# Optimization experiments

Hardware: AMD Instinct MI355X
Metric: run time of the kernel (lower is better)

## Reference

```python
import jax, jax.numpy as jnp
import numpy as np
import math

B, S, D, H = 8, 2048, 1024, 16
DH = D // H  # attention head size = 64

def setup_inputs() -> dict:
    key = jax.random.key(0)
    ks = jax.random.split(key, 10)
    s = 1.0 / math.sqrt(D)
    return {
        "hidden_states": jax.random.normal(ks[0], (B, S, D), dtype=jnp.float32),
        "attention_mask": jnp.zeros((B, 1, S), dtype=jnp.float32),
        "Wq": jax.random.normal(ks[1], (D, D), dtype=jnp.float32) * s,
        "bq": jnp.zeros((D,), dtype=jnp.float32),
        "Wqa": jax.random.normal(ks[2], (D, H), dtype=jnp.float32) * s,
        "bqa": jnp.zeros((H,), dtype=jnp.float32),
        "Wk": jax.random.normal(ks[3], (D, D), dtype=jnp.float32) * s,
        "bk": jnp.zeros((D,), dtype=jnp.float32),
        "Wt": jax.random.normal(ks[4], (D, D), dtype=jnp.float32) * s,
        "bt": jnp.zeros((D,), dtype=jnp.float32),
    }

def reference(hidden_states, attention_mask, Wq, bq, Wqa, bqa, Wk, bk, Wt, bt):
    scale = 1.0 / math.sqrt(DH)
    q = hidden_states @ Wq + bq                      # [B,S,D] mixed_query_layer
    k = hidden_states @ Wk + bk                      # [B,S,D] mixed_key_layer
    # query attention logits -> [B,H,S]
    q_score = jnp.swapaxes(q @ Wqa + bqa, 1, 2) * scale + attention_mask
    q_weight = jax.nn.softmax(q_score, axis=-1)      # [B,H,S]
    ql = jnp.swapaxes(q.reshape(B, S, H, DH), 1, 2)  # [B,H,S,DH]
    kl = jnp.swapaxes(k.reshape(B, S, H, DH), 1, 2)  # [B,H,S,DH]
    pooled_q = jnp.einsum('bhs,bhsd->bhd', q_weight, ql)          # [B,H,DH]
    qk_score = jnp.einsum('bhsd,bhd->bhs', kl, pooled_q) * scale + attention_mask
    qk_weight = jax.nn.softmax(qk_score, axis=-1)                 # [B,H,S]
    pooled_k = jnp.einsum('bhs,bhsd->bhd', qk_weight, kl)         # [B,H,DH]
    weighted = pooled_k[:, :, None, :] * ql                       # [B,H,S,DH]
    weighted = jnp.swapaxes(weighted, 1, 2).reshape(B, S, D)      # [B,S,D]
    out = weighted @ Wt + bt + q                                  # transform + residual to query
    return out
```

## Files before the change

kernel.cpp:

```cpp
#include <hip/hip_runtime.h>
#include <hip/hip_bf16.h>
#include <math.h>

#define BB 8
#define SS 2048
#define DD 1024
#define HH 16
#define DHH 64
#define NROWS (BB*SS)
#define QSLICE ((size_t)BB * HH * SS)

typedef unsigned short u16;
typedef __attribute__((ext_vector_type(8))) __bf16 bf16x8;
typedef __attribute__((ext_vector_type(4))) float f32x4;

__device__ __forceinline__ u16 f2bf(float f) {
    union { float f; unsigned u; } v; v.f = f;
    unsigned r = v.u + 0x7fffu + ((v.u >> 16) & 1u);
    return (u16)(r >> 16);
}
__device__ __forceinline__ float bf2f(u16 b) {
    union { unsigned u; float f; } v; v.u = ((unsigned)b) << 16;
    return v.f;
}

__device__ __forceinline__ void load_lds16(const void* g, void* l) {
    __builtin_amdgcn_global_load_lds(
        (const __attribute__((address_space(1))) unsigned int*)g,
        (__attribute__((address_space(3))) unsigned int*)l,
        16, 0, 0);
}

#define BAR() do { asm volatile("" ::: "memory"); \
                   __builtin_amdgcn_s_barrier();  \
                   asm volatile("" ::: "memory"); } while (0)

__global__ __launch_bounds__(256) void cast_bf16_kernel(const float* __restrict__ in,
                                                        u16* __restrict__ out, int n4) {
    int i = blockIdx.x * 256 + threadIdx.x;
    if (i >= n4) return;
    float4 v = ((const float4*)in)[i];
    ushort4 o;
    o.x = f2bf(v.x); o.y = f2bf(v.y); o.z = f2bf(v.z); o.w = f2bf(v.w);
    ((ushort4*)out)[i] = o;
}

__global__ __launch_bounds__(256) void transpose_cast_kernel(const float* __restrict__ W,
                                                             u16* __restrict__ WT) {
    __shared__ float tile[32][33];
    int m0 = blockIdx.x * 32, k0 = blockIdx.y * 32;
    int tx = threadIdx.x & 31, ty = threadIdx.x >> 5;
    #pragma unroll
    for (int i = 0; i < 4; i++) {
        int kk = ty + i * 8;
        tile[kk][tx] = W[(k0 + kk) * DD + m0 + tx];
    }
    __syncthreads();
    #pragma unroll
    for (int i = 0; i < 4; i++) {
        int mm = ty + i * 8;
        WT[(m0 + mm) * DD + k0 + tx] = f2bf(tile[tx][mm]);
    }
}

__global__ __launch_bounds__(256) void wqa_transpose_kernel(const float* __restrict__ Wqa,
                                                            u16* __restrict__ WqaT) {
    int i = blockIdx.x * 256 + threadIdx.x;
    int h = i >> 10, k = i & 1023;
    WqaT[i] = f2bf(Wqa[k * HH + h]);
}

template<int MODE>
__global__ __launch_bounds__(512, 2)
void gemm256_kernel(const u16* __restrict__ A, const u16* __restrict__ BT,
                    const float* __restrict__ b0, const float* __restrict__ b1,
                    const u16* __restrict__ res, float* __restrict__ Cf,
                    u16* __restrict__ C0, u16* __restrict__ C1) {
    __shared__ u16 smem[69632];
    const int by = blockIdx.y;
    const int row0 = blockIdx.x * 256;
    const int bcol0 = by * 256;
    const int colg0 = (MODE == 1) ? (bcol0 & 1023) : bcol0;
    const float* bias = (MODE == 1 && by >= 4) ? b1 : b0;
    u16* Cb = (MODE == 1 && by >= 4) ? C1 : C0;

    const int t = threadIdx.x;
    const int w = t >> 6, lane = t & 63;
    const int wm = w >> 2, wn = w & 3;
    const int m16 = lane & 15, quad = lane >> 4;

    f32x4 acc[8][4];
    #pragma unroll
    for (int i = 0; i < 8; i++)
        #pragma unroll
        for (int j = 0; j < 4; j++)
            acc[i][j] = (f32x4){0.f, 0.f, 0.f, 0.f};

    const int srow = t >> 3;
    const int scol = ((t & 7) ^ (srow & 7)) * 8;
    const u16* Ag = A + (size_t)(row0 + srow) * DD + scol;
    const u16* Bg = BT + (size_t)(bcol0 + srow) * DD + scol;

    auto STAGE_H = [&](int ktile, int mat, int half) {
        if (ktile >= 16) return;
        const int buf = ktile & 1;
        const int k0 = ktile * 64;
        const u16* g = mat ? Bg : Ag;
        u16* s = smem + mat * 32768 + buf * 16384;
        #pragma unroll
        for (int j = 0; j < 2; ++j)
            load_lds16(g + k0 + (size_t)(half * 128 + j * 64) * DD,
                       s + half * 8192 + j * 4096 + t * 8);
    };

    STAGE_H(0, 0, 0); STAGE_H(0, 0, 1); STAGE_H(0, 1, 0); STAGE_H(0, 1, 1);
    STAGE_H(1, 0, 0);
    asm volatile("s_waitcnt vmcnt(2)" ::: "memory");
    BAR();

    for (int kt = 0; kt < 16; ++kt) {
        const int cur = kt & 1;
        const u16* sAc = smem + cur * 16384;
        const u16* sBc = smem + 32768 + cur * 16384;
        bf16x8 af[4][2], bfr[4][2];

        #pragma unroll
        for (int mi = 0; mi < 4; ++mi)
            #pragma unroll
            for (int ks = 0; ks < 2; ++ks)
                af[mi][ks] = *(const bf16x8*)&sAc[(wm * 128 + mi * 16 + m16) * 64 +
                                                 (((ks * 4 + quad) ^ (m16 & 7)) * 8)];
        #pragma unroll
        for (int ni = 0; ni < 2; ++ni)
            #pragma unroll
            for (int ks = 0; ks < 2; ++ks)
                bfr[ni][ks] = *(const bf16x8*)&sBc[(wn * 64 + ni * 16 + m16) * 64 +
                                                   (((ks * 4 + quad) ^ (m16 & 7)) * 8)];
        STAGE_H(kt + 1, 0, 1);
        BAR();
        __builtin_amdgcn_s_setprio(1);
        #pragma unroll
        for (int mi = 0; mi < 4; ++mi)
            #pragma unroll
            for (int ni = 0; ni < 2; ++ni)
                #pragma unroll
                for (int ks = 0; ks < 2; ++ks)
                    acc[mi][ni] = __builtin_amdgcn_mfma_f32_16x16x32_bf16(
                        bfr[ni][ks], af[mi][ks], acc[mi][ni], 0, 0, 0);
        __builtin_amdgcn_s_setprio(0);
        BAR();

        #pragma unroll
        for (int ni = 2; ni < 4; ++ni)
            #pragma unroll
            for (int ks = 0; ks < 2; ++ks)
                bfr[ni][ks] = *(const bf16x8*)&sBc[(wn * 64 + ni * 16 + m16) * 64 +
                                                   (((ks * 4 + quad) ^ (m16 & 7)) * 8)];
        STAGE_H(kt + 1, 1, 0);
        BAR();
        __builtin_amdgcn_s_setprio(1);
        #pragma unroll
        for (int mi = 0; mi < 4; ++mi)
            #pragma unroll
            for (int ni = 2; ni < 4; ++ni)
                #pragma unroll
                for (int ks = 0; ks < 2; ++ks)
                    acc[mi][ni] = __builtin_amdgcn_mfma_f32_16x16x32_bf16(
                        bfr[ni][ks], af[mi][ks], acc[mi][ni], 0, 0, 0);
        __builtin_amdgcn_s_setprio(0);
        BAR();

        #pragma unroll
        for (int mi = 0; mi < 4; ++mi)
            #pragma unroll
            for (int ks = 0; ks < 2; ++ks)
                af[mi][ks] = *(const bf16x8*)&sAc[(wm * 128 + (4 + mi) * 16 + m16) * 64 +
                                                 (((ks * 4 + quad) ^ (m16 & 7)) * 8)];
        STAGE_H(kt + 1, 1, 1);
        BAR();
        __builtin_amdgcn_s_setprio(1);
        #pragma unroll
        for (int mi = 0; mi < 4; ++mi)
            #pragma unroll
            for (int ni = 0; ni < 2; ++ni)
                #pragma unroll
                for (int ks = 0; ks < 2; ++ks)
                    acc[4 + mi][ni] = __builtin_amdgcn_mfma_f32_16x16x32_bf16(
                        bfr[ni][ks], af[mi][ks], acc[4 + mi][ni], 0, 0, 0);
        __builtin_amdgcn_s_setprio(0);
        BAR();

        STAGE_H(kt + 2, 0, 0);
        BAR();
        __builtin_amdgcn_s_setprio(1);
        #pragma unroll
        for (int mi = 0; mi < 4; ++mi)
            #pragma unroll
            for (int ni = 2; ni < 4; ++ni)
                #pragma unroll
                for (int ks = 0; ks < 2; ++ks)
                    acc[4 + mi][ni] = __builtin_amdgcn_mfma_f32_16x16x32_bf16(
                        bfr[ni][ks], af[mi][ks], acc[4 + mi][ni], 0, 0, 0);
        __builtin_amdgcn_s_setprio(0);
        if (kt < 14) asm volatile("s_waitcnt vmcnt(2)" ::: "memory");
        else         asm volatile("s_waitcnt vmcnt(0)" ::: "memory");
        BAR();
    }

    u16* sC = smem;
    #pragma unroll
    for (int mi = 0; mi < 8; ++mi) {
        const int lrow = wm * 128 + mi * 16 + m16;
        #pragma unroll
        for (int ni = 0; ni < 4; ++ni) {
            const int lcol = wn * 64 + ni * 16 + quad * 4;
            const float4 bv = *(const float4*)&bias[colg0 + lcol];
            if (MODE == 1) {
                ushort4 o;
                o.x = f2bf(acc[mi][ni][0] + bv.x);
                o.y = f2bf(acc[mi][ni][1] + bv.y);
                o.z = f2bf(acc[mi][ni][2] + bv.z);
                o.w = f2bf(acc[mi][ni][3] + bv.w);
                *(ushort4*)&sC[(size_t)lrow * 272 + lcol] = o;
            } else {
                const size_t idx = (size_t)(row0 + lrow) * DD + colg0 + lcol;
                const ushort4 rv = *(const ushort4*)&res[idx];
                float4 o;
                o.x = acc[mi][ni][0] + bv.x + bf2f(rv.x);
                o.y = acc[mi][ni][1] + bv.y + bf2f(rv.y);
                o.z = acc[mi][ni][2] + bv.z + bf2f(rv.z);
                o.w = acc[mi][ni][3] + bv.w + bf2f(rv.w);
                *(float4*)&Cf[idx] = o;
            }
        }
    }
    if (MODE == 1) {
        __syncthreads();
        #pragma unroll
        for (int it = 0; it < 16; ++it) {
            const int r = it * 16 + (t >> 5);
            const int c = t & 31;
            uint4 v = *(const uint4*)&sC[(size_t)r * 272 + c * 8];
            *(uint4*)&Cb[(size_t)(row0 + r) * DD + colg0 + c * 8] = v;
        }
    }
}

__global__ __launch_bounds__(256)
void qscore_mfma_kernel(const u16* __restrict__ qbf, const u16* __restrict__ WqaT,
                        float* __restrict__ qraw) {
    int w = threadIdx.x >> 6, lane = threadIdx.x & 63;
    int row0 = blockIdx.x * 64 + w * 16;
    int kbase = blockIdx.y * 256;
    int m16 = lane & 15, quad = lane >> 4;
    f32x4 acc = (f32x4){0.f, 0.f, 0.f, 0.f};
    const u16* ap = qbf + (size_t)(row0 + m16) * DD + kbase + quad * 8;
    const u16* bp = WqaT + (size_t)m16 * DD + kbase + quad * 8;
    #pragma unroll
    for (int kk = 0; kk < 256; kk += 32) {
        bf16x8 a = *(const bf16x8*)(ap + kk);
        bf16x8 b = *(const bf16x8*)(bp + kk);
        acc = __builtin_amdgcn_mfma_f32_16x16x32_bf16(a, b, acc, 0, 0, 0);
    }
    #pragma unroll
    for (int r = 0; r < 4; r++) {
        int grow = row0 + quad * 4 + r;
        int b = grow >> 11, sidx = grow & 2047;
        qraw[((size_t)(blockIdx.y * BB + b) * HH + m16) * SS + sidx] = acc[r];
    }
}

template<bool EPI>
__global__ __launch_bounds__(256)
void softmax_kernel(float* __restrict__ score, const float* __restrict__ bqa,
                    const float* __restrict__ mask) {
    int bh = blockIdx.x;
    int b = bh >> 4, h = bh & 15;
    float* srow = score + ((size_t)bh << 11);
    __shared__ float rm[4], rs[4];
    int t = threadIdx.x;

    float v[8];
    float m = -1e30f;
    #pragma unroll
    for (int i = 0; i < 8; i++) {
        int off = t + i * 256;
        float x;
        if (EPI) {
            x = srow[off] + srow[off + QSLICE] + srow[off + 2 * QSLICE] + srow[off + 3 * QSLICE];
            x = (x + bqa[h]) * 0.125f + mask[b * SS + off];
        } else {
            x = srow[off];
        }
        v[i] = x; m = fmaxf(m, x);
    }
    #pragma unroll
    for (int off = 32; off; off >>= 1) m = fmaxf(m, __shfl_xor(m, off));
    if ((t & 63) == 0) rm[t >> 6] = m;
    __syncthreads();
    m = fmaxf(fmaxf(rm[0], rm[1]), fmaxf(rm[2], rm[3]));

    float sum = 0.f;
    #pragma unroll
    for (int i = 0; i < 8; i++) { v[i] = __expf(v[i] - m); sum += v[i]; }
    #pragma unroll
    for (int off = 32; off; off >>= 1) sum += __shfl_xor(sum, off);
    if ((t & 63) == 0) rs[t >> 6] = sum;
    __syncthreads();
    float inv = 1.0f / (rs[0] + rs[1] + rs[2] + rs[3]);
    #pragma unroll
    for (int i = 0; i < 8; i++) srow[t + i * 256] = v[i] * inv;
}

__global__ __launch_bounds__(256)
void pool_kernel(const float* __restrict__ w, const u16* __restrict__ X,
                 float* __restrict__ pooled) {
    int b = blockIdx.x;
    int s0 = blockIdx.y * 32;
    int t = threadIdx.x;
    int wid = t >> 6, lane = t & 63;
    int h = lane >> 2;
    __shared__ float sw[16 * 33];
    __shared__ float pr[4][64 * 17];
    {
        int hh = t >> 4, si = t & 15;
        const float* wr = w + ((size_t)(b * HH + hh) << 11) + s0;
        sw[hh * 33 + si] = wr[si];
        sw[hh * 33 + si + 16] = wr[si + 16];
    }
    __syncthreads();
    float acc[16];
    #pragma unroll
    for (int j = 0; j < 16; j++) acc[j] = 0.f;
    const u16* xbase = X + ((size_t)(b * SS + s0 + wid * 8) << 10) + lane * 16;
    #pragma unroll
    for (int rr = 0; rr < 8; rr++) {
        float ws = sw[h * 33 + wid * 8 + rr];
        const uint4* xp = (const uint4*)(xbase + (size_t)rr * DD);
        uint4 x0 = xp[0], x1 = xp[1];
        unsigned xw[8] = {x0.x, x0.y, x0.z, x0.w, x1.x, x1.y, x1.z, x1.w};
        #pragma unroll
        for (int i2 = 0; i2 < 8; i2++) {
            union { unsigned u; float f; } lo, hi;
            lo.u = xw[i2] << 16; hi.u = xw[i2] & 0xffff0000u;
            acc[2 * i2]     += ws * lo.f;
            acc[2 * i2 + 1] += ws * hi.f;
        }
    }
    #pragma unroll
    for (int j = 0; j < 16; j++) pr[wid][lane * 17 + j] = acc[j];
    __syncthreads();
    #pragma unroll
    for (int i = 0; i < 4; i++) {
        int idx = t + i * 256;
        int l2 = idx >> 4, j2 = idx & 15;
        float v = pr[0][l2 * 17 + j2] + pr[1][l2 * 17 + j2] +
                  pr[2][l2 * 17 + j2] + pr[3][l2 * 17 + j2];
        int od = (l2 >> 2) * 64 + (l2 & 3) * 16 + j2;
        atomicAdd(&pooled[b * DD + od], v);
    }
}

__global__ __launch_bounds__(256)
void qkscore_kernel(const u16* __restrict__ kbf, const float* __restrict__ pq,
                    const float* __restrict__ mask, float* __restrict__ qkscore) {
    int row = blockIdx.x * 4 + (threadIdx.x >> 6);
    int lane = threadIdx.x & 63;
    int b = row >> 11, s = row & 2047;
    int h = lane >> 2, dp = lane & 3;
    const u16* kp = kbf + (size_t)row * DD + h * 64 + dp * 16;
    const float* pqp = pq + (size_t)(b * HH + h) * 64 + dp * 16;
    const uint4* kp4 = (const uint4*)kp;
    uint4 ka = kp4[0], kb4 = kp4[1];
    unsigned kw[8] = {ka.x, ka.y, ka.z, ka.w, kb4.x, kb4.y, kb4.z, kb4.w};
    float acc = 0.f;
    #pragma unroll
    for (int i = 0; i < 8; i++) {
        union { unsigned u; float f; } lo, hi;
        lo.u = kw[i] << 16;
        hi.u = kw[i] & 0xffff0000u;
        acc += lo.f * pqp[2 * i] + hi.f * pqp[2 * i + 1];
    }
    acc += __shfl_xor(acc, 1);
    acc += __shfl_xor(acc, 2);
    if (dp == 0) qkscore[(size_t)(b * HH + h) * SS + s] = acc * 0.125f + mask[b * SS + s];
}

__global__ __launch_bounds__(256)
void weighted_kernel(const u16* __restrict__ qbf, const float* __restrict__ pk,
                     u16* __restrict__ wout) {
    int i = blockIdx.x * 256 + threadIdx.x;
    int row = i >> 8;
    int c0 = (i & 255) << 2;
    int b = row >> 11;
    int h = c0 >> 6, d = c0 & 63;
    ushort4 qv = ((const ushort4*)qbf)[i];
    const float4 pv = *(const float4*)(pk + (size_t)(b * HH + h) * 64 + d);
    ushort4 o;
    o.x = f2bf(bf2f(qv.x) * pv.x); o.y = f2bf(bf2f(qv.y) * pv.y);
    o.z = f2bf(bf2f(qv.z) * pv.z); o.w = f2bf(bf2f(qv.w) * pv.w);
    ((ushort4*)wout)[i] = o;
}

extern "C" void kernel_launch(void* const* d_in, const int* in_sizes, int n_in,
                              void* d_out, int out_size, void* d_ws, size_t ws_size,
                              hipStream_t stream) {
    const float* hs   = (const float*)d_in[0];
    const float* mask = (const float*)d_in[1];
    const float* Wq   = (const float*)d_in[2];
    const float* bq   = (const float*)d_in[3];
    const float* Wqa  = (const float*)d_in[4];
    const float* bqa  = (const float*)d_in[5];
    const float* Wk   = (const float*)d_in[6];
    const float* bk   = (const float*)d_in[7];
    const float* Wt   = (const float*)d_in[8];
    const float* bt   = (const float*)d_in[9];
    float* out = (float*)d_out;

    char* ws = (char*)d_ws;
    u16*   hs_bf = (u16*)ws;   ws += (size_t)NROWS * DD * 2;
    u16*   WqT   = (u16*)ws;   ws += (size_t)DD * DD * 2;
    u16*   WkT   = (u16*)ws;   ws += (size_t)DD * DD * 2;
    u16*   WtT   = (u16*)ws;   ws += (size_t)DD * DD * 2;
    u16*   WqaT  = (u16*)ws;   ws += (size_t)HH * DD * 2;
    u16*   q_bf  = (u16*)ws;   ws += (size_t)NROWS * DD * 2;
    u16*   k_bf  = (u16*)ws;   ws += (size_t)NROWS * DD * 2;
    float* qraw  = (float*)ws; ws += QSLICE * 4 * 4;
    float* qksc  = (float*)ws; ws += (size_t)BB * HH * SS * 4;
    float* pq    = (float*)ws; ws += (size_t)BB * HH * 64 * 4;
    float* pk    = (float*)ws; ws += (size_t)BB * HH * 64 * 4;
    u16*   wbf   = hs_bf;

    int n4 = NROWS * DD / 4;
    cast_bf16_kernel<<<n4 / 256, 256, 0, stream>>>(hs, hs_bf, n4);
    transpose_cast_kernel<<<dim3(32, 32), 256, 0, stream>>>(Wq, WqT);
    transpose_cast_kernel<<<dim3(32, 32), 256, 0, stream>>>(Wk, WkT);
    transpose_cast_kernel<<<dim3(32, 32), 256, 0, stream>>>(Wt, WtT);
    wqa_transpose_kernel<<<HH * DD / 256, 256, 0, stream>>>(Wqa, WqaT);

    hipMemsetAsync(pq, 0, (size_t)BB * HH * 64 * 4, stream);
    hipMemsetAsync(pk, 0, (size_t)BB * HH * 64 * 4, stream);

    gemm256_kernel<1><<<dim3(NROWS / 256, 8), 512, 0, stream>>>(
        hs_bf, WqT, bq, bk, nullptr, nullptr, q_bf, k_bf);

    qscore_mfma_kernel<<<dim3(NROWS / 64, 4), 256, 0, stream>>>(q_bf, WqaT, qraw);
    softmax_kernel<true><<<BB * HH, 256, 0, stream>>>(qraw, bqa, mask);
    pool_kernel<<<dim3(BB, SS / 32), 256, 0, stream>>>(qraw, q_bf, pq);
    qkscore_kernel<<<NROWS / 4, 256, 0, stream>>>(k_bf, pq, mask, qksc);
    softmax_kernel<false><<<BB * HH, 256, 0, stream>>>(qksc, nullptr, nullptr);
    pool_kernel<<<dim3(BB, SS / 32), 256, 0, stream>>>(qksc, k_bf, pk);
    weighted_kernel<<<n4 / 256, 256, 0, stream>>>(q_bf, pk, wbf);

    gemm256_kernel<2><<<dim3(NROWS / 256, 4), 512, 0, stream>>>(
        wbf, WtT, bt, nullptr, q_bf, out, nullptr, nullptr);
}
```

Baseline: 309.6 us.

## Fold pooled-key scaling into per-batch Wt, fuse q-score into QK GEMM, merge prep kernels

Replaces the elementwise weighted = pk*q pass with a per-batch scaled copy of WtT, so the output GEMM reads q_bf directly against batch-specific weights. The q@Wqa logits are now computed in the QK GEMM epilogue from the bf16 q tile already in LDS, which removes the separate qscore kernel and its reread of q. The casts, transposes and memsets are merged into one prep kernel to cut launch overhead. In exchange it writes 8 scaled weight copies (16 MB), and the output GEMM's B-operand reuse across batches drops.

```diff
diff --git a/kernel.cpp b/kernel.cpp
--- a/kernel.cpp
+++ b/kernel.cpp
@@ -35,39 +35,57 @@
                    __builtin_amdgcn_s_barrier();  \
                    asm volatile("" ::: "memory"); } while (0)
 
-__global__ __launch_bounds__(256) void cast_bf16_kernel(const float* __restrict__ in,
-                                                        u16* __restrict__ out, int n4) {
-    int i = blockIdx.x * 256 + threadIdx.x;
-    if (i >= n4) return;
-    float4 v = ((const float4*)in)[i];
-    ushort4 o;
-    o.x = f2bf(v.x); o.y = f2bf(v.y); o.z = f2bf(v.z); o.w = f2bf(v.w);
-    ((ushort4*)out)[i] = o;
-}
-
-__global__ __launch_bounds__(256) void transpose_cast_kernel(const float* __restrict__ W,
-                                                             u16* __restrict__ WT) {
+__global__ __launch_bounds__(256)
+void prep_kernel(const float* __restrict__ hs, u16* __restrict__ hs_bf,
+                 const float* __restrict__ Wq, u16* __restrict__ WqT,
+                 const float* __restrict__ Wk, u16* __restrict__ WkT,
+                 const float* __restrict__ Wt, u16* __restrict__ WtT,
+                 const float* __restrict__ Wqa, u16* __restrict__ WqaT,
+                 float* __restrict__ pq, float* __restrict__ pk) {
     __shared__ float tile[32][33];
-    int m0 = blockIdx.x * 32, k0 = blockIdx.y * 32;
-    int tx = threadIdx.x & 31, ty = threadIdx.x >> 5;
-    #pragma unroll
-    for (int i = 0; i < 4; i++) {
-        int kk = ty + i * 8;
-        tile[kk][tx] = W[(k0 + kk) * DD + m0 + tx];
-    }
-    __syncthreads();
-    #pragma unroll
-    for (int i = 0; i < 4; i++) {
-        int mm = ty + i * 8;
-        WT[(m0 + mm) * DD + k0 + tx] = f2bf(tile[tx][mm]);
-    }
-}
-
-__global__ __launch_bounds__(256) void wqa_transpose_kernel(const float* __restrict__ Wqa,
-                                                            u16* __restrict__ WqaT) {
-    int i = blockIdx.x * 256 + threadIdx.x;
-    int h = i >> 10, k = i & 1023;
-    WqaT[i] = f2bf(Wqa[k * HH + h]);
+    const int bid = blockIdx.x;
+    const int t = threadIdx.x;
+    if (bid < 16384) {
+        int i = bid * 256 + t;
+        float4 v = ((const float4*)hs)[i];
+        ushort4 o;
+        o.x = f2bf(v.x); o.y = f2bf(v.y); o.z = f2bf(v.z); o.w = f2bf(v.w);
+        ((ushort4*)hs_bf)[i] = o;
+        return;
+    }
+    if (bid < 19456) {
+        int rel = bid - 16384;
+        const float* W; u16* WT;
+        if (rel < 1024)      { W = Wq; WT = WqT; }
+        else if (rel < 2048) { W = Wk; WT = WkT; rel -= 1024; }
+        else                 { W = Wt; WT = WtT; rel -= 2048; }
+        int m0 = (rel & 31) * 32, k0 = (rel >> 5) * 32;
+        int tx = t & 31, ty = t >> 5;
+        #pragma unroll
+        for (int i = 0; i < 4; i++) {
+            int kk = ty + i * 8;
+            tile[kk][tx] = W[(k0 + kk) * DD + m0 + tx];
+        }
+        __syncthreads();
+        #pragma unroll
+        for (int i = 0; i < 4; i++) {
+            int mm = ty + i * 8;
+            WT[(m0 + mm) * DD + k0 + tx] = f2bf(tile[tx][mm]);
+        }
+        return;
+    }
+    if (bid < 19520) {
+        int i = (bid - 19456) * 256 + t;
+        int h = i >> 10, k = i & 1023;
+        WqaT[i] = f2bf(Wqa[k * HH + h]);
+        return;
+    }
+    {
+        int i = (bid - 19520) * 256 + t;
+        float4 z = {0.f, 0.f, 0.f, 0.f};
+        if (i < 2048) ((float4*)pq)[i] = z;
+        else          ((float4*)pk)[i - 2048] = z;
+    }
 }
 
 template<int MODE>
@@ -75,7 +93,8 @@
 void gemm256_kernel(const u16* __restrict__ A, const u16* __restrict__ BT,
                     const float* __restrict__ b0, const float* __restrict__ b1,
                     const u16* __restrict__ res, float* __restrict__ Cf,
-                    u16* __restrict__ C0, u16* __restrict__ C1) {
+                    u16* __restrict__ C0, u16* __restrict__ C1,
+                    const u16* __restrict__ WqaT, float* __restrict__ qraw) {
     __shared__ u16 smem[69632];
     const int by = blockIdx.y;
     const int row0 = blockIdx.x * 256;
@@ -83,6 +102,7 @@
     const int colg0 = (MODE == 1) ? (bcol0 & 1023) : bcol0;
     const float* bias = (MODE == 1 && by >= 4) ? b1 : b0;
     u16* Cb = (MODE == 1 && by >= 4) ? C1 : C0;
+    const u16* BTb = (MODE == 2) ? BT + ((size_t)(row0 >> 11) << 20) : BT;
 
     const int t = threadIdx.x;
     const int w = t >> 6, lane = t & 63;
@@ -99,7 +119,7 @@
     const int srow = t >> 3;
     const int scol = ((t & 7) ^ (srow & 7)) * 8;
     const u16* Ag = A + (size_t)(row0 + srow) * DD + scol;
-    const u16* Bg = BT + (size_t)(bcol0 + srow) * DD + scol;
+    const u16* Bg = BTb + (size_t)(bcol0 + srow) * DD + scol;
 
     auto STAGE_H = [&](int ktile, int mat, int half) {
         if (ktile >= 16) return;
@@ -243,31 +263,50 @@
             uint4 v = *(const uint4*)&sC[(size_t)r * 272 + c * 8];
             *(uint4*)&Cb[(size_t)(row0 + r) * DD + colg0 + c * 8] = v;
         }
+        if (by < 4) {
+            const int bIdx = row0 >> 11;
+            bf16x8 wq[8];
+            const u16* bp = WqaT + (size_t)m16 * DD + by * 256 + quad * 8;
+            #pragma unroll
+            for (int kk = 0; kk < 8; ++kk) wq[kk] = *(const bf16x8*)(bp + kk * 32);
+            #pragma unroll
+            for (int rt = 0; rt < 2; ++rt) {
+                const int sr = (w * 2 + rt) * 16;
+                f32x4 qa = (f32x4){0.f, 0.f, 0.f, 0.f};
+                #pragma unroll
+                for (int kk = 0; kk < 8; ++kk) {
+                    bf16x8 a = *(const bf16x8*)&sC[(size_t)(sr + m16) * 272 + quad * 8 + kk * 32];
+                    qa = __builtin_amdgcn_mfma_f32_16x16x32_bf16(a, wq[kk], qa, 0, 0, 0);
+                }
+                #pragma unroll
+                for (int r = 0; r < 4; ++r) {
+                    int s = (row0 & 2047) + sr + quad * 4 + r;
+                    qraw[((size_t)(by * BB + bIdx) * HH + m16) * SS + s] = qa[r];
+                }
+            }
+        }
     }
 }
 
 __global__ __launch_bounds__(256)
-void qscore_mfma_kernel(const u16* __restrict__ qbf, const u16* __restrict__ WqaT,
-                        float* __restrict__ qraw) {
-    int w = threadIdx.x >> 6, lane = threadIdx.x & 63;
-    int row0 = blockIdx.x * 64 + w * 16;
-    int kbase = blockIdx.y * 256;
-    int m16 = lane & 15, quad = lane >> 4;
-    f32x4 acc = (f32x4){0.f, 0.f, 0.f, 0.f};
-    const u16* ap = qbf + (size_t)(row0 + m16) * DD + kbase + quad * 8;
-    const u16* bp = WqaT + (size_t)m16 * DD + kbase + quad * 8;
-    #pragma unroll
-    for (int kk = 0; kk < 256; kk += 32) {
-        bf16x8 a = *(const bf16x8*)(ap + kk);
-        bf16x8 b = *(const bf16x8*)(bp + kk);
-        acc = __builtin_amdgcn_mfma_f32_16x16x32_bf16(a, b, acc, 0, 0, 0);
-    }
-    #pragma unroll
-    for (int r = 0; r < 4; r++) {
-        int grow = row0 + quad * 4 + r;
-        int b = grow >> 11, sidx = grow & 2047;
-        qraw[((size_t)(blockIdx.y * BB + b) * HH + m16) * SS + sidx] = acc[r];
-    }
+void wtscale_kernel(const u16* __restrict__ WtT, const float* __restrict__ pk,
+                    u16* __restrict__ WtT8) {
+    size_t i = (size_t)blockIdx.x * 256 + threadIdx.x;
+    int b = (int)(i >> 17);
+    size_t off = (i & 131071) << 3;
+    int d = (int)(off & 1023);
+    const float4 p0 = *(const float4*)&pk[b * 1024 + d];
+    const float4 p1 = *(const float4*)&pk[b * 1024 + d + 4];
+    ushort4 a0 = ((const ushort4*)(WtT + off))[0];
+    ushort4 a1 = ((const ushort4*)(WtT + off))[1];
+    ushort4 o0, o1;
+    o0.x = f2bf(bf2f(a0.x) * p0.x); o0.y = f2bf(bf2f(a0.y) * p0.y);
+    o0.z = f2bf(bf2f(a0.z) * p0.z); o0.w = f2bf(bf2f(a0.w) * p0.w);
+    o1.x = f2bf(bf2f(a1.x) * p1.x); o1.y = f2bf(bf2f(a1.y) * p1.y);
+    o1.z = f2bf(bf2f(a1.z) * p1.z); o1.w = f2bf(bf2f(a1.w) * p1.w);
+    u16* dst = WtT8 + ((size_t)b << 20) + off;
+    ((ushort4*)dst)[0] = o0;
+    ((ushort4*)dst)[1] = o1;
 }
 
 template<bool EPI>
@@ -386,22 +425,6 @@
     if (dp == 0) qkscore[(size_t)(b * HH + h) * SS + s] = acc * 0.125f + mask[b * SS + s];
 }
 
-__global__ __launch_bounds__(256)
-void weighted_kernel(const u16* __restrict__ qbf, const float* __restrict__ pk,
-                     u16* __restrict__ wout) {
-    int i = blockIdx.x * 256 + threadIdx.x;
-    int row = i >> 8;
-    int c0 = (i & 255) << 2;
-    int b = row >> 11;
-    int h = c0 >> 6, d = c0 & 63;
-    ushort4 qv = ((const ushort4*)qbf)[i];
-    const float4 pv = *(const float4*)(pk + (size_t)(b * HH + h) * 64 + d);
-    ushort4 o;
-    o.x = f2bf(bf2f(qv.x) * pv.x); o.y = f2bf(bf2f(qv.y) * pv.y);
-    o.z = f2bf(bf2f(qv.z) * pv.z); o.w = f2bf(bf2f(qv.w) * pv.w);
-    ((ushort4*)wout)[i] = o;
-}
-
 extern "C" void kernel_launch(void* const* d_in, const int* in_sizes, int n_in,
                               void* d_out, int out_size, void* d_ws, size_t ws_size,
                               hipStream_t stream) {
@@ -429,29 +452,21 @@
     float* qksc  = (float*)ws; ws += (size_t)BB * HH * SS * 4;
     float* pq    = (float*)ws; ws += (size_t)BB * HH * 64 * 4;
     float* pk    = (float*)ws; ws += (size_t)BB * HH * 64 * 4;
-    u16*   wbf   = hs_bf;
-
-    int n4 = NROWS * DD / 4;
-    cast_bf16_kernel<<<n4 / 256, 256, 0, stream>>>(hs, hs_bf, n4);
-    transpose_cast_kernel<<<dim3(32, 32), 256, 0, stream>>>(Wq, WqT);
-    transpose_cast_kernel<<<dim3(32, 32), 256, 0, stream>>>(Wk, WkT);
-    transpose_cast_kernel<<<dim3(32, 32), 256, 0, stream>>>(Wt, WtT);
-    wqa_transpose_kernel<<<HH * DD / 256, 256, 0, stream>>>(Wqa, WqaT);
-
-    hipMemsetAsync(pq, 0, (size_t)BB * HH * 64 * 4, stream);
-    hipMemsetAsync(pk, 0, (size_t)BB * HH * 64 * 4, stream);
+    u16*   WtT8  = hs_bf;
+
+    prep_kernel<<<19536, 256, 0, stream>>>(hs, hs_bf, Wq, WqT, Wk, WkT, Wt, WtT,
+                                           Wqa, WqaT, pq, pk);
 
     gemm256_kernel<1><<<dim3(NROWS / 256, 8), 512, 0, stream>>>(
-        hs_bf, WqT, bq, bk, nullptr, nullptr, q_bf, k_bf);
-
-    qscore_mfma_kernel<<<dim3(NROWS / 64, 4), 256, 0, stream>>>(q_bf, WqaT, qraw);
+        hs_bf, WqT, bq, bk, nullptr, nullptr, q_bf, k_bf, WqaT, qraw);
+
     softmax_kernel<true><<<BB * HH, 256, 0, stream>>>(qraw, bqa, mask);
     pool_kernel<<<dim3(BB, SS / 32), 256, 0, stream>>>(qraw, q_bf, pq);
     qkscore_kernel<<<NROWS / 4, 256, 0, stream>>>(k_bf, pq, mask, qksc);
     softmax_kernel<false><<<BB * HH, 256, 0, stream>>>(qksc, nullptr, nullptr);
     pool_kernel<<<dim3(BB, SS / 32), 256, 0, stream>>>(qksc, k_bf, pk);
-    weighted_kernel<<<n4 / 256, 256, 0, stream>>>(q_bf, pk, wbf);
+    wtscale_kernel<<<4096, 256, 0, stream>>>(WtT, pk, WtT8);
 
     gemm256_kernel<2><<<dim3(NROWS / 256, 4), 512, 0, stream>>>(
-        wbf, WtT, bt, nullptr, q_bf, out, nullptr, nullptr);
-}
+        q_bf, WtT8, bt, nullptr, q_bf, out, nullptr, nullptr, nullptr, nullptr);
+}
```

Result: faster. 287.4 us (-7.2%).
